# Kernel optimization log

Hardware: AMD Instinct MI355X
Metric: run time of the kernel (lower is better)

The kernel has to match this reference:

```python
import jax, jax.numpy as jnp
import numpy as np

B, S, IN, H, Q, M, K = 32, 2048, 128, 256, 16, 64, 3


def setup_inputs() -> dict:
    key = jax.random.key(0)
    ks = jax.random.split(key, 12)
    rn = lambda k, shp, s=0.05: (jax.random.normal(k, shp, jnp.float32) * s)
    return {
        "input_sequence": rn(ks[0], (B, S, IN), 1.0),
        "W_ih0": rn(ks[1], (4 * H, IN)),
        "W_hh0": rn(ks[2], (4 * H, H)),
        "b_ih0": jnp.zeros((4 * H,), jnp.float32),
        "b_hh0": jnp.zeros((4 * H,), jnp.float32),
        "W_ih1": rn(ks[3], (4 * H, H)),
        "W_hh1": rn(ks[4], (4 * H, H)),
        "b_ih1": jnp.zeros((4 * H,), jnp.float32),
        "b_hh1": jnp.zeros((4 * H,), jnp.float32),
        "W_cq": rn(ks[5], (Q, H)),
        "b_cq": jnp.zeros((Q,), jnp.float32),
        "mem_keys": rn(ks[6], (M, Q), 1.0),
        "mem_vals": rn(ks[7], (M, H), 1.0),
        "W_out": rn(ks[8], (H, 2 * H)),
        "b_out": jnp.zeros((H,), jnp.float32),
        "classical_weight": jnp.float32(0.7),
        "quantum_weight": jnp.float32(0.3),
    }


def _lstm_layer(x, W_ih, W_hh, b_ih, b_hh):
    """PyTorch-convention LSTM layer (gate order i,f,g,o), batch_first input."""
    Bb = x.shape[0]
    Hh = W_hh.shape[1]
    # precompute the input contribution for all timesteps: [B,S,4H]
    xg = jnp.einsum('bsi,gi->bsg', x, W_ih) + b_ih + b_hh

    def step(carry, xt):
        h, c = carry
        g = xt + h @ W_hh.T  # [B,4H]
        i, f, gg, o = jnp.split(g, 4, axis=-1)
        i = jax.nn.sigmoid(i)
        f = jax.nn.sigmoid(f)
        gg = jnp.tanh(gg)
        o = jax.nn.sigmoid(o)
        c = f * c + i * gg
        h = o * jnp.tanh(c)
        return (h, c), h

    init = (jnp.zeros((Bb, Hh), x.dtype), jnp.zeros((Bb, Hh), x.dtype))
    _, hs = jax.lax.scan(step, init, jnp.swapaxes(xg, 0, 1))  # [S,B,H]
    return jnp.swapaxes(hs, 0, 1)


def _forward(input_sequence, W_ih0, W_hh0, b_ih0, b_hh0, W_ih1, W_hh1, b_ih1,
             b_hh1, W_cq, b_cq, mem_keys, mem_vals, W_out, b_out,
             classical_weight, quantum_weight):
    # classical 2-layer LSTM
    h1 = _lstm_layer(input_sequence, W_ih0, W_hh0, b_ih0, b_hh0)
    lstm_out = _lstm_layer(h1, W_ih1, W_hh1, b_ih1, b_hh1)  # [B,S,H]

    # classical_to_quantum + tanh -> per-token query [B,S,Q]
    q = jnp.tanh(jnp.einsum('bsh,qh->bsq', lstm_out, W_cq) + b_cq)

    # batched k-NN read over the quantum memory (cosine similarity, k=3)
    eps = jnp.float32(1e-8)
    qn = q / (jnp.linalg.norm(q, axis=-1, keepdims=True) + eps)
    kn = mem_keys / (jnp.linalg.norm(mem_keys, axis=-1, keepdims=True) + eps)
    sims = jnp.einsum('bsq,mq->bsm', qn, kn)          # [B,S,M]
    top_vals, top_idx = jax.lax.top_k(sims, K)        # [B,S,K]
    gathered = mem_vals[top_idx]                      # [B,S,K,H]

    # similarity-weighted average of retrieved contents
    tot = jnp.sum(top_vals, axis=-1, keepdims=True)   # [B,S,1]
    weighted = jnp.einsum('bsk,bskh->bsh', top_vals, gathered)
    enhanced = jnp.where(tot > 0, weighted / jnp.where(tot == 0, 1.0, tot), 0.0)

    # combine streams and project
    combined = jnp.concatenate(
        [classical_weight * lstm_out, quantum_weight * enhanced], axis=-1)
    out = jnp.einsum('bsc,hc->bsh', combined, W_out) + b_out  # [B,S,H]
    return out


def reference(input_sequence, W_ih0, W_hh0, b_ih0, b_hh0, W_ih1, W_hh1, b_ih1,
              b_hh1, W_cq, b_cq, mem_keys, mem_vals, W_out, b_out,
              classical_weight, quantum_weight):
    return _forward(input_sequence, W_ih0, W_hh0, b_ih0, b_hh0, W_ih1, W_hh1,
                    b_ih1, b_hh1, W_cq, b_cq, mem_keys, mem_vals, W_out, b_out,
                    classical_weight, quantum_weight)
```

## Files before the change

kernel.cpp:

```cpp
#include <hip/hip_runtime.h>
#include <cstdint>
#include <cstddef>
#include <math.h>

#define B_   32
#define S_   2048
#define IN_  128
#define H_   256
#define Q_   16
#define M_   64
#define D_   4

typedef unsigned long long u64;

__device__ __forceinline__ float4 ld4(const float* p) { return *(const float4*)p; }

#define AGLD64(p)    __hip_atomic_load((p),  __ATOMIC_RELAXED, __HIP_MEMORY_SCOPE_AGENT)
#define AGST64(p, v) __hip_atomic_store((p), (v), __ATOMIC_RELAXED, __HIP_MEMORY_SCOPE_AGENT)

__device__ __forceinline__ float sigm_f(float x) { return 1.0f / (1.0f + __expf(-x)); }
__device__ __forceinline__ float tanh_f(float x) { return 1.0f - 2.0f / (__expf(2.0f * x) + 1.0f); }

__global__ __launch_bounds__(256, 1) void lstm2(
    const float* __restrict__ x,
    const float* __restrict__ Wih0, const float* __restrict__ bih0,
    const float* __restrict__ bhh0, const float* __restrict__ Whh0,
    const float* __restrict__ Wih1, const float* __restrict__ bih1,
    const float* __restrict__ bhh1, const float* __restrict__ Whh1,
    float* __restrict__ out,
    u64* __restrict__ exs,
    u64* __restrict__ exf)
{
  const int f = blockIdx.x;
  const int n = f >> 5;
  const int b = f & 31;

  const int tid = threadIdx.x;
  const int w   = tid >> 6;
  const int l   = tid & 63;
  const int kc  = l & 7;
  const int rg  = l >> 3;
  const int wrg = w * 8 + rg;
  const int col = n * 32 + wrg;

  __shared__ float w1[128][257];
  __shared__ float aring[8][256];
  __shared__ float hring[2][256];
  __shared__ float x_sh[2][IN_];

#pragma unroll
  for (int s2 = 0; s2 < 8; s2++) aring[s2][tid] = 0.0f;
  hring[0][tid] = 0.0f;
  hring[1][tid] = 0.0f;

  float4 wf0[4][8], wf1[4][8], wi0[4][4];
  float rb0[4], rb1[4];
#pragma unroll
  for (int g = 0; g < 4; g++) {
    const int row = g * 256 + col;
    const float* p0 = Whh0 + (size_t)row * 256 + 4 * kc;
    const float* p1 = Whh1 + (size_t)row * 256 + 4 * kc;
    const float* pi = Wih0 + (size_t)row * 128 + 4 * kc;
#pragma unroll
    for (int j = 0; j < 8; j++) {
      wf0[g][j] = ld4(p0 + 32 * j);
      wf1[g][j] = ld4(p1 + 32 * j);
    }
#pragma unroll
    for (int j = 0; j < 4; j++) wi0[g][j] = ld4(pi + 32 * j);
    rb0[g] = bih0[row] + bhh0[row];
    rb1[g] = bih1[row] + bhh1[row];
    const float* pw = Wih1 + (size_t)row * 256 + 4 * kc;
    float* dst = &w1[g * 32 + wrg][4 * kc];
#pragma unroll
    for (int j = 0; j < 8; j++) *(float4*)(dst + 32 * j) = ld4(pw + 32 * j);
  }

  const float* xrow = x + (size_t)b * S_ * IN_;
  float* outp = out + (size_t)b * S_ * H_;
  u64* sexb = exs + (size_t)b * 1024;
  volatile u64* fexb = (volatile u64*)(exf + (size_t)b * 1024);

  if (tid < IN_) {
    x_sh[0][tid] = xrow[tid];
    x_sh[1][tid] = xrow[IN_ + tid];
  }
  float xreg = (tid < IN_) ? xrow[(size_t)2 * IN_ + tid] : 0.0f;
  float cst0 = 0.0f, cst1 = 0.0f;
  float xa0s[4], xa1s[4] = {0, 0, 0, 0};
  __syncthreads();

  {
    const float* xb = x_sh[0];
    float4 xv[4];
#pragma unroll
    for (int j = 0; j < 4; j++) xv[j] = ld4(xb + 4 * kc + 32 * j);
#pragma unroll
    for (int g = 0; g < 4; g++) {
      float4 s4 = {0, 0, 0, 0};
#pragma unroll
      for (int j = 0; j < 4; j++) {
        s4.x += wi0[g][j].x * xv[j].x; s4.y += wi0[g][j].y * xv[j].y;
        s4.z += wi0[g][j].z * xv[j].z; s4.w += wi0[g][j].w * xv[j].w;
      }
      float s = (s4.x + s4.y) + (s4.z + s4.w);
      s += __shfl_xor(s, 1); s += __shfl_xor(s, 2); s += __shfl_xor(s, 4);
      xa0s[g] = s + rb0[g];
    }
  }

  const bool own = ((tid >> 5) == n);
  bool dead = false;
  for (int t = 0; t < S_ + D_; ++t) {
    const bool doA = (t < S_);
    const int  u   = t - D_;
    const bool doH = (u >= 0);
    const int  pa = t & 1, ph = u & 1;

    if (doA) {
      const float* ap = aring[(t - 1) & 7];
      float4 av[8];
#pragma unroll
      for (int j = 0; j < 8; j++) av[j] = ld4(ap + 4 * kc + 32 * j);
      float gv[4];
#pragma unroll
      for (int g = 0; g < 4; g++) {
        float4 s4 = {0, 0, 0, 0};
#pragma unroll
        for (int j = 0; j < 8; j++) {
          s4.x += wf0[g][j].x * av[j].x; s4.y += wf0[g][j].y * av[j].y;
          s4.z += wf0[g][j].z * av[j].z; s4.w += wf0[g][j].w * av[j].w;
        }
        float s = (s4.x + s4.y) + (s4.z + s4.w);
        s += __shfl_xor(s, 1); s += __shfl_xor(s, 2); s += __shfl_xor(s, 4);
        gv[g] = s + xa0s[g];
      }
      float ig = sigm_f(gv[0]);
      float fg = sigm_f(gv[1]);
      float cg = tanh_f(gv[2]);
      float og = sigm_f(gv[3]);
      cst0 = fg * cst0 + ig * cg;
      float a = og * tanh_f(cst0);
      if (kc == 0) {
        u64 pk = ((u64)(unsigned)(t + 1) << 32) | (u64)__float_as_uint(a);
        fexb[((0 * 2 + pa) << 8) + col] = pk;
        AGST64(sexb + ((0 * 2 + pa) << 8) + col, pk);
        aring[t & 7][col] = a;
      }
    }
    if (doH) {
      const float* hp = hring[(t - 1) & 1];
      float4 hv[8];
#pragma unroll
      for (int j = 0; j < 8; j++) hv[j] = ld4(hp + 4 * kc + 32 * j);
      float gv[4];
#pragma unroll
      for (int g = 0; g < 4; g++) {
        float4 s4 = {0, 0, 0, 0};
#pragma unroll
        for (int j = 0; j < 8; j++) {
          s4.x += wf1[g][j].x * hv[j].x; s4.y += wf1[g][j].y * hv[j].y;
          s4.z += wf1[g][j].z * hv[j].z; s4.w += wf1[g][j].w * hv[j].w;
        }
        float s = (s4.x + s4.y) + (s4.z + s4.w);
        s += __shfl_xor(s, 1); s += __shfl_xor(s, 2); s += __shfl_xor(s, 4);
        gv[g] = s + xa1s[g];
      }
      float ig = sigm_f(gv[0]);
      float fg = sigm_f(gv[1]);
      float cg = tanh_f(gv[2]);
      float og = sigm_f(gv[3]);
      cst1 = fg * cst1 + ig * cg;
      float h = og * tanh_f(cst1);
      if (kc == 0) {
        outp[(size_t)u * H_ + col] = h;
        u64 pk = ((u64)(unsigned)(u + 1) << 32) | (u64)__float_as_uint(h);
        fexb[((1 * 2 + ph) << 8) + col] = pk;
        AGST64(sexb + ((1 * 2 + ph) << 8) + col, pk);
        hring[u & 1][col] = h;
      }
    }

    bool needA = doA && !own && !dead;
    bool needH = doH && !own && !dead;
    const unsigned eA = (unsigned)(t + 1), eH = (unsigned)(u + 1);
    volatile u64* fA = fexb + ((0 * 2 + pa) << 8) + tid;
    volatile u64* fH = fexb + ((1 * 2 + ph) << 8) + tid;
    u64 vA = 0, vH = 0;
    if (needA) vA = *fA;
    if (needH) vH = *fH;

    if (t + 1 < S_) {
      const float* xb = x_sh[(t + 1) & 1];
      float4 xv[4];
#pragma unroll
      for (int j = 0; j < 4; j++) xv[j] = ld4(xb + 4 * kc + 32 * j);
#pragma unroll
      for (int g = 0; g < 4; g++) {
        float4 s4 = {0, 0, 0, 0};
#pragma unroll
        for (int j = 0; j < 4; j++) {
          s4.x += wi0[g][j].x * xv[j].x; s4.y += wi0[g][j].y * xv[j].y;
          s4.z += wi0[g][j].z * xv[j].z; s4.w += wi0[g][j].w * xv[j].w;
        }
        float s = (s4.x + s4.y) + (s4.z + s4.w);
        s += __shfl_xor(s, 1); s += __shfl_xor(s, 2); s += __shfl_xor(s, 4);
        xa0s[g] = s + rb0[g];
      }
    }
    {
      const int v = t - D_ + 1;
      if (v >= 0 && v < S_) {
        const float* avp = aring[v & 7];
        float4 av[8];
#pragma unroll
        for (int j = 0; j < 8; j++) av[j] = ld4(avp + 4 * kc + 32 * j);
#pragma unroll
        for (int g = 0; g < 4; g++) {
          const float* wr = &w1[g * 32 + wrg][4 * kc];
          float4 s4 = {0, 0, 0, 0};
#pragma unroll
          for (int j = 0; j < 8; j++) {
            float4 wv = ld4(wr + 32 * j);
            s4.x += wv.x * av[j].x; s4.y += wv.y * av[j].y;
            s4.z += wv.z * av[j].z; s4.w += wv.w * av[j].w;
          }
          float s = (s4.x + s4.y) + (s4.z + s4.w);
          s += __shfl_xor(s, 1); s += __shfl_xor(s, 2); s += __shfl_xor(s, 4);
          xa1s[g] = s + rb1[g];
        }
      }
    }
    float xreg_n = 0.0f;
    if (tid < IN_ && t + 2 < S_) {
      int tn = (t + 3 < S_) ? t + 3 : S_ - 1;
      xreg_n = xrow[(size_t)tn * IN_ + tid];
    }

    if (needA && (unsigned)(vA >> 32) == eA) needA = false;
    if (needH && (unsigned)(vH >> 32) == eH) needH = false;
#pragma unroll 1
    for (int spin = 0; (needA || needH) && spin < 6; ++spin) {
      if (needA) { vA = *fA; if ((unsigned)(vA >> 32) == eA) needA = false; }
      if (needH) { vH = *fH; if ((unsigned)(vH >> 32) == eH) needH = false; }
    }
    if (needA || needH) {
      u64* sA = sexb + ((0 * 2 + pa) << 8) + tid;
      u64* sH = sexb + ((1 * 2 + ph) << 8) + tid;
      unsigned guard = 0;
      while (needA || needH) {
        if (needA) { vA = AGLD64(sA); if ((unsigned)(vA >> 32) == eA) needA = false; }
        if (needH) { vH = AGLD64(sH); if ((unsigned)(vH >> 32) == eH) needH = false; }
        if (++guard >= (1u << 20)) { dead = true; break; }
      }
    }
    if (doA && !own) aring[t & 7][tid] = __uint_as_float((unsigned)vA);
    if (doH && !own) hring[u & 1][tid] = __uint_as_float((unsigned)vH);

    if (tid < IN_ && t < S_) x_sh[t & 1][tid] = xreg;
    xreg = xreg_n;
    __syncthreads();
  }
}

__global__ __launch_bounds__(256) void knn_enh(
    const float* __restrict__ lstm, const float* __restrict__ Wcq,
    const float* __restrict__ bcq, const float* __restrict__ keys,
    const float* __restrict__ vals, const float* __restrict__ qwp,
    float* __restrict__ enh)
{
  const int tid  = threadIdx.x;
  const int wave = tid >> 6, lane = tid & 63;
  const int t = blockIdx.x * 4 + wave;

  __shared__ float xsh[4][256];
  __shared__ float qsh[4][16];

  const float* xrow = lstm + (size_t)t * H_;
  float4 x4 = ld4(xrow + lane * 4);
  *(float4*)&xsh[wave][lane * 4] = x4;
  __syncthreads();

  const int j = lane & 15, seg = lane >> 4;
  const float* wrow = Wcq + j * H_ + seg * 64;
  const float* xseg = &xsh[wave][seg * 64];
  float p = 0.0f;
#pragma unroll
  for (int c = 0; c < 64; c += 4) {
    float4 w4 = ld4(wrow + c);
    p += w4.x * xseg[c] + w4.y * xseg[c + 1] + w4.z * xseg[c + 2] + w4.w * xseg[c + 3];
  }
  p += __shfl_xor(p, 16);
  p += __shfl_xor(p, 32);
  float q = tanhf(p + bcq[j]);

  float sq = q * q;
  sq += __shfl_xor(sq, 1); sq += __shfl_xor(sq, 2);
  sq += __shfl_xor(sq, 4); sq += __shfl_xor(sq, 8);
  float qn = q / (sqrtf(sq) + 1e-8f);
  if (lane < 16) qsh[wave][lane] = qn;
  __syncthreads();

  const int m = lane;
  const float* krow = keys + m * Q_;
  float kv[16]; float kn2 = 0.0f;
#pragma unroll
  for (int jj = 0; jj < 16; jj++) { kv[jj] = krow[jj]; kn2 += kv[jj] * kv[jj]; }
  float rn = 1.0f / (sqrtf(kn2) + 1e-8f);
  float sim = 0.0f;
#pragma unroll
  for (int jj = 0; jj < 16; jj++) sim += qsh[wave][jj] * kv[jj];
  sim *= rn;

  float rem = sim;
  float tv[3]; int ti[3];
#pragma unroll
  for (int k = 0; k < 3; k++) {
    float v = rem; int idx = m;
#pragma unroll
    for (int d = 1; d < 64; d <<= 1) {
      float ov = __shfl_xor(v, d);
      int   oi = __shfl_xor(idx, d);
      if (ov > v || (ov == v && oi < idx)) { v = ov; idx = oi; }
    }
    tv[k] = v; ti[k] = idx;
    if (m == idx) rem = -INFINITY;
  }
  float tot = tv[0] + tv[1] + tv[2];

  float ex = 0, ey = 0, ez = 0, ew = 0;
#pragma unroll
  for (int k = 0; k < 3; k++) {
    float4 vv = ld4(vals + (size_t)ti[k] * H_ + lane * 4);
    ex += tv[k] * vv.x; ey += tv[k] * vv.y;
    ez += tv[k] * vv.z; ew += tv[k] * vv.w;
  }
  float inv = (tot > 0.0f) ? 1.0f / tot : 0.0f;
  const float qw = qwp[0];

  float4 o;
  o.x = qw * ex * inv; o.y = qw * ey * inv;
  o.z = qw * ez * inv; o.w = qw * ew * inv;
  *(float4*)&enh[(size_t)t * H_ + lane * 4] = o;
}

__global__ __launch_bounds__(256) void gemm_cat(
    float* __restrict__ io, const float* __restrict__ A2,
    const float* __restrict__ Bw, const float* __restrict__ bias,
    const float* __restrict__ cwp)
{
  __shared__ float As[16][68];
  __shared__ float Bs[16][260];
  const int tid  = threadIdx.x;
  const int row0 = blockIdx.x * 64;
  const int tx = tid & 15, ty = tid >> 4;
  const int lr = tid >> 2;
  const int lk = (tid & 3) << 2;
  const float cw = cwp[0];

  float acc[4][16];
#pragma unroll
  for (int i = 0; i < 4; i++)
#pragma unroll
    for (int j = 0; j < 16; j++) acc[i][j] = 0.0f;

  for (int k0 = 0; k0 < 512; k0 += 16) {
    float4 av;
    if (k0 < 256) {
      av = ld4(io + (size_t)(row0 + lr) * 256 + k0 + lk);
      av.x *= cw; av.y *= cw; av.z *= cw; av.w *= cw;
    } else {
      av = ld4(A2 + (size_t)(row0 + lr) * 256 + (k0 - 256) + lk);
    }
    As[lk + 0][lr] = av.x; As[lk + 1][lr] = av.y;
    As[lk + 2][lr] = av.z; As[lk + 3][lr] = av.w;
    const float* bp = Bw + (size_t)tid * 512 + k0;
#pragma unroll
    for (int q = 0; q < 4; q++) {
      float4 b4 = ld4(bp + 4 * q);
      Bs[4 * q + 0][tid] = b4.x; Bs[4 * q + 1][tid] = b4.y;
      Bs[4 * q + 2][tid] = b4.z; Bs[4 * q + 3][tid] = b4.w;
    }
    __syncthreads();
#pragma unroll
    for (int k = 0; k < 16; k++) {
      float4 a4 = *(const float4*)&As[k][ty << 2];
      float aa[4] = {a4.x, a4.y, a4.z, a4.w};
#pragma unroll
      for (int cc = 0; cc < 4; cc++) {
        float4 b4 = *(const float4*)&Bs[k][cc * 64 + (tx << 2)];
        float bb[4] = {b4.x, b4.y, b4.z, b4.w};
#pragma unroll
        for (int i = 0; i < 4; i++)
#pragma unroll
          for (int jj = 0; jj < 4; jj++) acc[i][cc * 4 + jj] += aa[i] * bb[jj];
      }
    }
    __syncthreads();
  }

#pragma unroll
  for (int i = 0; i < 4; i++) {
#pragma unroll
    for (int cc = 0; cc < 4; cc++) {
      int c0 = cc * 64 + (tx << 2);
      float4 o;
      o.x = acc[i][cc * 4 + 0] + bias[c0 + 0];
      o.y = acc[i][cc * 4 + 1] + bias[c0 + 1];
      o.z = acc[i][cc * 4 + 2] + bias[c0 + 2];
      o.w = acc[i][cc * 4 + 3] + bias[c0 + 3];
      *(float4*)&io[(size_t)(row0 + (ty << 2) + i) * 256 + c0] = o;
    }
  }
}

extern "C" void kernel_launch(void* const* d_in, const int* in_sizes, int n_in,
                              void* d_out, int out_size, void* d_ws, size_t ws_size,
                              hipStream_t stream)
{
  const float* x    = (const float*)d_in[0];
  const float* Wih0 = (const float*)d_in[1];
  const float* Whh0 = (const float*)d_in[2];
  const float* bih0 = (const float*)d_in[3];
  const float* bhh0 = (const float*)d_in[4];
  const float* Wih1 = (const float*)d_in[5];
  const float* Whh1 = (const float*)d_in[6];
  const float* bih1 = (const float*)d_in[7];
  const float* bhh1 = (const float*)d_in[8];
  const float* Wcq  = (const float*)d_in[9];
  const float* bcq  = (const float*)d_in[10];
  const float* keys = (const float*)d_in[11];
  const float* vals = (const float*)d_in[12];
  const float* Wout = (const float*)d_in[13];
  const float* bout = (const float*)d_in[14];
  const float* cw   = (const float*)d_in[15];
  const float* qw   = (const float*)d_in[16];
  float* out = (float*)d_out;

  const size_t HE = (size_t)B_ * S_ * H_;
  if (ws_size < HE * sizeof(float)) return;
  u64* exs = (u64*)d_ws;
  u64* exf = exs + (size_t)32 * 1024;
  float* enh = (float*)d_ws;

  const int MT = B_ * S_;
  dim3 blk(256);

  hipMemsetAsync(exs, 0, (size_t)2 * 32 * 1024 * sizeof(u64), stream);
  lstm2<<<dim3(256), blk, 0, stream>>>(x, Wih0, bih0, bhh0, Whh0,
                                       Wih1, bih1, bhh1, Whh1, out, exs, exf);

  knn_enh<<<dim3(MT / 4), blk, 0, stream>>>(out, Wcq, bcq, keys, vals, qw, enh);

  gemm_cat<<<dim3(MT / 64), blk, 0, stream>>>(out, enh, Wout, bout, cw);
}
```

Baseline: 15.89 ms.

## Poll cross-block LSTM exchange with cache-bypassing 128-bit loads on a single buffer

Removes the separate volatile fast-path exchange buffer and its duplicate stores, keeping only the agent-scope atomic buffer. Each waiting thread now polls two adjacent tagged entries at once with an inline-asm global_load_dwordx4 carrying sc0 sc1 bits, meant to read past the local caches, and only falls back to per-entry atomic loads after 16 tries. Threads 0-127 handle the layer-0 exchange and 128-255 the layer-1 exchange in parallel, where before every thread waited on both. The x prefetch moves to the top of the step. The goal is lower per-timestep synchronization latency, at the risk that the asm's coherence bits are incorrect, or that polling with explicit waitcnt takes longer in practice.

```diff
diff --git a/kernel.cpp b/kernel.cpp
--- a/kernel.cpp
+++ b/kernel.cpp
@@ -12,11 +12,19 @@
 #define D_   4
 
 typedef unsigned long long u64;
+typedef __attribute__((ext_vector_type(4))) unsigned int u32x4;
 
 __device__ __forceinline__ float4 ld4(const float* p) { return *(const float4*)p; }
 
 #define AGLD64(p)    __hip_atomic_load((p),  __ATOMIC_RELAXED, __HIP_MEMORY_SCOPE_AGENT)
 #define AGST64(p, v) __hip_atomic_store((p), (v), __ATOMIC_RELAXED, __HIP_MEMORY_SCOPE_AGENT)
+
+__device__ __forceinline__ u32x4 mall_load_2x64(const u64* p) {
+  u32x4 q;
+  asm volatile("global_load_dwordx4 %0, %1, off sc0 sc1\n\ts_waitcnt vmcnt(0)"
+               : "=v"(q) : "v"(p) : "memory");
+  return q;
+}
 
 __device__ __forceinline__ float sigm_f(float x) { return 1.0f / (1.0f + __expf(-x)); }
 __device__ __forceinline__ float tanh_f(float x) { return 1.0f - 2.0f / (__expf(2.0f * x) + 1.0f); }
@@ -28,8 +36,7 @@
     const float* __restrict__ Wih1, const float* __restrict__ bih1,
     const float* __restrict__ bhh1, const float* __restrict__ Whh1,
     float* __restrict__ out,
-    u64* __restrict__ exs,
-    u64* __restrict__ exf)
+    u64* __restrict__ exs)
 {
   const int f = blockIdx.x;
   const int n = f >> 5;
@@ -79,7 +86,6 @@
   const float* xrow = x + (size_t)b * S_ * IN_;
   float* outp = out + (size_t)b * S_ * H_;
   u64* sexb = exs + (size_t)b * 1024;
-  volatile u64* fexb = (volatile u64*)(exf + (size_t)b * 1024);
 
   if (tid < IN_) {
     x_sh[0][tid] = xrow[tid];
@@ -109,13 +115,19 @@
     }
   }
 
-  const bool own = ((tid >> 5) == n);
   bool dead = false;
   for (int t = 0; t < S_ + D_; ++t) {
     const bool doA = (t < S_);
     const int  u   = t - D_;
     const bool doH = (u >= 0);
     const int  pa = t & 1, ph = u & 1;
+    const unsigned eA = (unsigned)(t + 1), eH = (unsigned)(u + 1);
+
+    float xreg_n = 0.0f;
+    if (tid < IN_ && t + 2 < S_) {
+      int tn = (t + 3 < S_) ? t + 3 : S_ - 1;
+      xreg_n = xrow[(size_t)tn * IN_ + tid];
+    }
 
     if (doA) {
       const float* ap = aring[(t - 1) & 7];
@@ -142,8 +154,7 @@
       cst0 = fg * cst0 + ig * cg;
       float a = og * tanh_f(cst0);
       if (kc == 0) {
-        u64 pk = ((u64)(unsigned)(t + 1) << 32) | (u64)__float_as_uint(a);
-        fexb[((0 * 2 + pa) << 8) + col] = pk;
+        u64 pk = ((u64)eA << 32) | (u64)__float_as_uint(a);
         AGST64(sexb + ((0 * 2 + pa) << 8) + col, pk);
         aring[t & 7][col] = a;
       }
@@ -174,21 +185,11 @@
       float h = og * tanh_f(cst1);
       if (kc == 0) {
         outp[(size_t)u * H_ + col] = h;
-        u64 pk = ((u64)(unsigned)(u + 1) << 32) | (u64)__float_as_uint(h);
-        fexb[((1 * 2 + ph) << 8) + col] = pk;
+        u64 pk = ((u64)eH << 32) | (u64)__float_as_uint(h);
         AGST64(sexb + ((1 * 2 + ph) << 8) + col, pk);
         hring[u & 1][col] = h;
       }
     }
-
-    bool needA = doA && !own && !dead;
-    bool needH = doH && !own && !dead;
-    const unsigned eA = (unsigned)(t + 1), eH = (unsigned)(u + 1);
-    volatile u64* fA = fexb + ((0 * 2 + pa) << 8) + tid;
-    volatile u64* fH = fexb + ((1 * 2 + ph) << 8) + tid;
-    u64 vA = 0, vH = 0;
-    if (needA) vA = *fA;
-    if (needH) vH = *fH;
 
     if (t + 1 < S_) {
       const float* xb = x_sh[(t + 1) & 1];
@@ -231,31 +232,40 @@
         }
       }
     }
-    float xreg_n = 0.0f;
-    if (tid < IN_ && t + 2 < S_) {
-      int tn = (t + 3 < S_) ? t + 3 : S_ - 1;
-      xreg_n = xrow[(size_t)tn * IN_ + tid];
-    }
-
-    if (needA && (unsigned)(vA >> 32) == eA) needA = false;
-    if (needH && (unsigned)(vH >> 32) == eH) needH = false;
+
+    {
+      const bool isA = (tid < 128);
+      const int  pi2 = isA ? tid : tid - 128;
+      const bool ownp = ((pi2 >> 4) == n);
+      const bool act  = isA ? doA : doH;
+      bool need = act && !ownp && !dead;
+      if (need) {
+        const unsigned etag = isA ? eA : eH;
+        const int plane = isA ? (0 * 2 + pa) : (1 * 2 + ph);
+        u64* base = sexb + (plane << 8) + 2 * pi2;
+        unsigned val0 = 0, val1 = 0;
+        bool got = false;
 #pragma unroll 1
-    for (int spin = 0; (needA || needH) && spin < 6; ++spin) {
-      if (needA) { vA = *fA; if ((unsigned)(vA >> 32) == eA) needA = false; }
-      if (needH) { vH = *fH; if ((unsigned)(vH >> 32) == eH) needH = false; }
-    }
-    if (needA || needH) {
-      u64* sA = sexb + ((0 * 2 + pa) << 8) + tid;
-      u64* sH = sexb + ((1 * 2 + ph) << 8) + tid;
-      unsigned guard = 0;
-      while (needA || needH) {
-        if (needA) { vA = AGLD64(sA); if ((unsigned)(vA >> 32) == eA) needA = false; }
-        if (needH) { vH = AGLD64(sH); if ((unsigned)(vH >> 32) == eH) needH = false; }
-        if (++guard >= (1u << 20)) { dead = true; break; }
-      }
-    }
-    if (doA && !own) aring[t & 7][tid] = __uint_as_float((unsigned)vA);
-    if (doH && !own) hring[u & 1][tid] = __uint_as_float((unsigned)vH);
+        for (int it = 0; it < 16 && !got; ++it) {
+          u32x4 q = mall_load_2x64(base);
+          if (q.y == etag && q.w == etag) { val0 = q.x; val1 = q.z; got = true; }
+        }
+        if (!got) {
+          bool g0 = false, g1 = false;
+          unsigned guard = 0;
+          while (!(g0 && g1)) {
+            if (!g0) { u64 v = AGLD64(base);     if ((unsigned)(v >> 32) == etag) { val0 = (unsigned)v; g0 = true; } }
+            if (!g1) { u64 v = AGLD64(base + 1); if ((unsigned)(v >> 32) == etag) { val1 = (unsigned)v; g1 = true; } }
+            if (++guard >= (1u << 20)) { dead = true; break; }
+          }
+        }
+        float2 f2;
+        f2.x = __uint_as_float(val0);
+        f2.y = __uint_as_float(val1);
+        if (isA) *(float2*)&aring[t & 7][2 * pi2] = f2;
+        else     *(float2*)&hring[u & 1][2 * pi2] = f2;
+      }
+    }
 
     if (tid < IN_ && t < S_) x_sh[t & 1][tid] = xreg;
     xreg = xreg_n;
@@ -440,15 +450,14 @@
   const size_t HE = (size_t)B_ * S_ * H_;
   if (ws_size < HE * sizeof(float)) return;
   u64* exs = (u64*)d_ws;
-  u64* exf = exs + (size_t)32 * 1024;
   float* enh = (float*)d_ws;
 
   const int MT = B_ * S_;
   dim3 blk(256);
 
-  hipMemsetAsync(exs, 0, (size_t)2 * 32 * 1024 * sizeof(u64), stream);
+  hipMemsetAsync(exs, 0, (size_t)32 * 1024 * sizeof(u64), stream);
   lstm2<<<dim3(256), blk, 0, stream>>>(x, Wih0, bih0, bhh0, Whh0,
-                                       Wih1, bih1, bhh1, Whh1, out, exs, exf);
+                                       Wih1, bih1, bhh1, Whh1, out, exs);
 
   knn_enh<<<dim3(MT / 4), blk, 0, stream>>>(out, Wcq, bcq, keys, vals, qw, enh);
 
```

Result: faster. 13.57 ms (-14.6%).
